# Performance work log

Hardware: AMD Instinct MI355X
Metric: run time of the kernel (lower is better)

The kernel has to match this reference:

```python
import jax, jax.numpy as jnp
import numpy as np

H = 8          # num heads
HD = 64        # head dim
DV = 512       # values_dim
DC = 128       # coords_dim
DI = 512       # att_inner_dim
DF = 2048      # mlp inner dim


def _ln(x, g, b, eps=1e-5):
    mu = jnp.mean(x, -1, keepdims=True)
    var = jnp.mean((x - mu) ** 2, -1, keepdims=True)
    return (x - mu) * jax.lax.rsqrt(var + eps) * g + b


def _rms(x, g, eps=1e-6):
    return x * jax.lax.rsqrt(jnp.mean(x * x, -1, keepdims=True) + eps) * g


def _heads(x):  # b n (h d) -> b h n d
    b, n, _ = x.shape
    return x.reshape(b, n, H, HD).transpose(0, 2, 1, 3)


def setup_inputs() -> dict:
    key = jax.random.key(0)
    ks = iter(jax.random.split(key, 40))
    r = lambda shape, s=0.02: jax.random.normal(next(ks), shape, jnp.float32) * s
    inp = {
        'coords': jax.random.normal(next(ks), (4, 4096, DC), jnp.float32),
        'values': jax.random.normal(next(ks), (4, 4096, DV), jnp.float32),
        'Lv': jax.random.normal(next(ks), (4, 1024, DV), jnp.float32),
        'Lc': jax.random.normal(next(ks), (4, 1024, DC), jnp.float32),
        'lam': jax.random.normal(next(ks), (1,), jnp.float32),
        'lvn_g': jnp.ones((DV,)), 'lvn_b': jnp.zeros((DV,)),
        'lcn_g': jnp.ones((DC,)), 'lcn_b': jnp.zeros((DC,)),
        'ck_w': r((DC, DI)), 'ck_b': jnp.zeros((DI,)), 'ck_g': jnp.ones((DI,)),
        'cq_w': r((DC, DI)), 'cq_b': jnp.zeros((DI,)), 'cq_g': jnp.ones((DI,)),
        'vq_w': r((DV, DI)), 'vq_b': jnp.zeros((DI,)), 'vq_g': jnp.ones((DI,)),
        'vk_w': r((DV, 2 * DI)), 'vk_b': jnp.zeros((2 * DI,)),
        'op_w': r((DI, DV)), 'op_b': jnp.zeros((DV,)),
        'oln_g': jnp.ones((DV,)), 'oln_b': jnp.zeros((DV,)),
        'm1_w': r((DV, DF)), 'm1_b': jnp.zeros((DF,)),
        'm2_w': r((DF, DF)), 'm2_b': jnp.zeros((DF,)),
        'm3_w': r((DF, DV)), 'm3_b': jnp.zeros((DV,)),
    }
    return inp


def reference(coords, values, Lv, Lc, lam, lvn_g, lvn_b, lcn_g, lcn_b,
              ck_w, ck_b, ck_g, cq_w, cq_b, cq_g, vq_w, vq_b, vq_g,
              vk_w, vk_b, op_w, op_b, oln_g, oln_b,
              m1_w, m1_b, m2_w, m2_b, m3_w, m3_b):
    Lv = _ln(Lv, lvn_g, lvn_b)
    Lc = _ln(Lc, lcn_g, lcn_b)
    vk = Lv @ vk_w + vk_b                     # [b, nl, 2*DI]
    v_v, k_v = jnp.split(vk, 2, axis=-1)
    k_c = _rms(Lc @ ck_w + ck_b, ck_g)
    k_c, v_v, k_v = _heads(k_c), _heads(v_v), _heads(k_v)  # [b,h,nl,d]
    q_v = _heads(_rms(values @ vq_w + vq_b, vq_g))         # [b,h,nq,d]
    q_c = _heads(_rms(coords @ cq_w + cq_b, cq_g))
    # dual-score attention
    scores = jnp.einsum('bhnd,bhmd->bhnm', q_c, k_c) \
        + lam[0] * jnp.einsum('bhnd,bhmd->bhnm', q_v, k_v)
    scores = scores / np.float32(np.sqrt(HD))
    attn = jax.nn.softmax(scores, axis=-1)
    V_out = jnp.einsum('bhnm,bhmd->bhnd', attn, v_v)       # [b,h,nq,d]
    b, _, nq, _ = V_out.shape
    V_out = V_out.transpose(0, 2, 1, 3).reshape(b, nq, DI)
    V_out = V_out @ op_w + op_b
    # (LayerNorm, MLP) head: Linear-GELU-Linear-GELU-Linear
    h = _ln(V_out, oln_g, oln_b)
    h = jax.nn.gelu(h @ m1_w + m1_b)
    h = jax.nn.gelu(h @ m2_w + m2_b)
    return h @ m3_w + m3_b
```

## Files before the change

### kernel.cpp

```cpp
#include <hip/hip_runtime.h>
#include <cstdint>
#include <cstddef>

typedef __bf16 bf16_t;
typedef __bf16 bf16x8 __attribute__((ext_vector_type(8)));
typedef __bf16 bf16x4 __attribute__((ext_vector_type(4)));
typedef __bf16 bf16x2 __attribute__((ext_vector_type(2)));
typedef float  f32x4  __attribute__((ext_vector_type(4)));

typedef __attribute__((address_space(1))) void gvoid_t;
typedef __attribute__((address_space(3))) void lvoid_t;

__device__ __forceinline__ f32x4 mfma16(bf16x8 a, bf16x8 b, f32x4 c) {
  return __builtin_amdgcn_mfma_f32_16x16x32_bf16(a, b, c, 0, 0, 0);
}

__device__ __forceinline__ void async_copy16(const void* g, void* l) {
  __builtin_amdgcn_global_load_lds((gvoid_t*)g, (lvoid_t*)l, 16, 0, 0);
}

__device__ __forceinline__ float gelu_tanh(float x) {
  float u = 0.7978845608028654f * (x + 0.044715f * x * x * x);
  float e = exp2f(2.8853900817779268f * u);
  float t = 1.f - 2.f / (e + 1.f);
  return 0.5f * x * (1.f + t);
}

struct TransBatch {
  const float* src[8];
  bf16_t* dst[8];
  int K[8], N[8], bx[8], base[8];
};

__global__ void transpose_batch_kernel(TransBatch d) {
  int id = blockIdx.x;
  int mi = 0;
#pragma unroll
  for (int j = 1; j < 8; j++)
    if (id >= d.base[j]) mi = j;
  int local = id - d.base[mi];
  int bxw = d.bx[mi];
  int n0 = (local % bxw) * 32, k0 = (local / bxw) * 32;
  const float* in = d.src[mi];
  bf16_t* out = d.dst[mi];
  int K = d.K[mi], N = d.N[mi];

  __shared__ float t[32][33];
  int tx = threadIdx.x, ty = threadIdx.y;
#pragma unroll
  for (int i = 0; i < 4; i++)
    t[ty + i * 8][tx] = in[(size_t)(k0 + ty + i * 8) * N + n0 + tx];
  __syncthreads();
#pragma unroll
  for (int i = 0; i < 4; i++)
    out[(size_t)(n0 + ty + i * 8) * K + k0 + tx] = (bf16_t)t[tx][ty + i * 8];
}

__global__ void transpose_v_kernel(const bf16_t* __restrict__ vk, bf16_t* __restrict__ vt) {
  __shared__ bf16_t t[32][33];
  int b = blockIdx.z;
  int d0 = blockIdx.x * 32, m0 = blockIdx.y * 32;
  int tx = threadIdx.x, ty = threadIdx.y;
#pragma unroll
  for (int i = 0; i < 4; i++)
    t[ty + i * 8][tx] = vk[((size_t)b * 1024 + m0 + ty + i * 8) * 1024 + d0 + tx];
  __syncthreads();
#pragma unroll
  for (int i = 0; i < 4; i++)
    vt[((size_t)b * 512 + d0 + ty + i * 8) * 1024 + m0 + tx] = t[tx][ty + i * 8];
}

__global__ void cvt2_bf16_kernel(const float* __restrict__ a, bf16_t* __restrict__ oa, int n4a,
                                 const float* __restrict__ b, bf16_t* __restrict__ ob, int n4b) {
  int i = blockIdx.x * blockDim.x + threadIdx.x;
  const float* s;
  bf16_t* o;
  int j;
  if (i < n4a) { s = a; o = oa; j = i; }
  else { j = i - n4a; if (j >= n4b) return; s = b; o = ob; }
  float4 v = ((const float4*)s)[j];
  bf16x4 r = {(bf16_t)v.x, (bf16_t)v.y, (bf16_t)v.z, (bf16_t)v.w};
  ((bf16x4*)o)[j] = r;
}

template <int D, bool IS_RMS, typename TI>
__global__ __launch_bounds__(256) void rownorm_kernel(
    const TI* __restrict__ x, const float* __restrict__ g,
    const float* __restrict__ bb, bf16_t* __restrict__ out) {
  constexpr int V = D / 64;
  const int row = blockIdx.x * 4 + (threadIdx.x >> 6);
  const int lane = threadIdx.x & 63;
  const size_t base = (size_t)row * D + (size_t)lane * V;
  float v[V];
  if constexpr (sizeof(TI) == 2) {
    bf16x8 xv = *(const bf16x8*)(x + base);
#pragma unroll
    for (int j = 0; j < V; j++) v[j] = (float)xv[j];
  } else if constexpr (V == 8) {
    float4 a = ((const float4*)(x + base))[0];
    float4 b2 = ((const float4*)(x + base))[1];
    v[0] = a.x; v[1] = a.y; v[2] = a.z; v[3] = a.w;
    v[4] = b2.x; v[5] = b2.y; v[6] = b2.z; v[7] = b2.w;
  } else {
    float2 a = *(const float2*)(x + base);
    v[0] = a.x; v[1] = a.y;
  }
  float s = 0.f, s2 = 0.f;
#pragma unroll
  for (int j = 0; j < V; j++) { s += v[j]; s2 += v[j] * v[j]; }
#pragma unroll
  for (int o = 32; o > 0; o >>= 1) { s += __shfl_xor(s, o); s2 += __shfl_xor(s2, o); }
  float mu, rr;
  if constexpr (IS_RMS) {
    mu = 0.f;
    rr = rsqrtf(s2 * (1.f / D) + 1e-6f);
  } else {
    mu = s * (1.f / D);
    rr = rsqrtf(s2 * (1.f / D) - mu * mu + 1e-5f);
  }
  float o[V];
#pragma unroll
  for (int j = 0; j < V; j++) {
    float gv = g[lane * V + j];
    float bv;
    if constexpr (IS_RMS) bv = 0.f; else bv = bb[lane * V + j];
    o[j] = (v[j] - mu) * rr * gv + bv;
  }
  if constexpr (V == 8) {
    bf16x8 ov;
#pragma unroll
    for (int j = 0; j < 8; j++) ov[j] = (bf16_t)o[j];
    *(bf16x8*)(out + base) = ov;
  } else {
    bf16x2 ov;
    ov[0] = (bf16_t)o[0]; ov[1] = (bf16_t)o[1];
    *(bf16x2*)(out + base) = ov;
  }
}

template <int EPI>
__global__ __launch_bounds__(256, 2) void gemm_bt(
    const bf16_t* __restrict__ A, const bf16_t* __restrict__ Bt,
    const float* __restrict__ bias, void* __restrict__ outp,
    int M, int N, int K) {
  __shared__ __align__(16) bf16_t As[128 * 64];
  __shared__ __align__(16) bf16_t Bs[128 * 64];
  const int tid = threadIdx.x;
  const int lane = tid & 63, wv = tid >> 6;
  const int quad = lane >> 4, l16 = lane & 15;
  int nwg = gridDim.x * gridDim.y;
  int bid = blockIdx.y * gridDim.x + blockIdx.x;
  if (!(nwg & 7)) { int cpx = nwg >> 3; bid = (bid & 7) * cpx + (bid >> 3); }
  const int m_base = (bid / gridDim.x) * 128, n_base = (bid % gridDim.x) * 128;
  const int wm = wv & 1, wn = wv >> 1;
  f32x4 acc[4][4] = {};

  for (int k0 = 0; k0 < K; k0 += 64) {
#pragma unroll
    for (int c = 0; c < 4; c++) {
      int p = c * 256 + tid;
      int row = p >> 3;
      int gc = (p & 7) ^ (row & 7);
      async_copy16(&A[(size_t)(m_base + row) * K + k0 + gc * 8], &As[(size_t)p * 8]);
      async_copy16(&Bt[(size_t)(n_base + row) * K + k0 + gc * 8], &Bs[(size_t)p * 8]);
    }
    __syncthreads();
#pragma unroll
    for (int ks = 0; ks < 2; ks++) {
      bf16x8 af[4], bfr[4];
#pragma unroll
      for (int mi = 0; mi < 4; mi++) {
        int r = wm * 64 + mi * 16 + l16;
        int c = (ks * 4 + quad) ^ (r & 7);
        af[mi] = *(const bf16x8*)&As[(size_t)(r * 8 + c) * 8];
      }
#pragma unroll
      for (int ni = 0; ni < 4; ni++) {
        int r = wn * 64 + ni * 16 + l16;
        int c = (ks * 4 + quad) ^ (r & 7);
        bfr[ni] = *(const bf16x8*)&Bs[(size_t)(r * 8 + c) * 8];
      }
#pragma unroll
      for (int mi = 0; mi < 4; mi++)
#pragma unroll
        for (int ni = 0; ni < 4; ni++)
          acc[mi][ni] = mfma16(af[mi], bfr[ni], acc[mi][ni]);
    }
    __syncthreads();
  }

#pragma unroll
  for (int mi = 0; mi < 4; mi++) {
    int m = m_base + wm * 64 + mi * 16 + quad * 4;
#pragma unroll
    for (int ni = 0; ni < 4; ni++) {
      int n = n_base + wn * 64 + ni * 16 + l16;
      float bv = bias[n];
#pragma unroll
      for (int r2 = 0; r2 < 4; r2++) {
        float v = acc[mi][ni][r2] + bv;
        if (EPI == 2) v = gelu_tanh(v);
        if (EPI == 0) ((float*)outp)[(size_t)(m + r2) * N + n] = v;
        else          ((bf16_t*)outp)[(size_t)(m + r2) * N + n] = (bf16_t)v;
      }
    }
  }
}

#define SF __builtin_amdgcn_sched_barrier(0)

template <int EPI>
__global__ __launch_bounds__(512, 2) void gemm256(
    const bf16_t* __restrict__ A, const bf16_t* __restrict__ Bt,
    const float* __restrict__ bias, void* __restrict__ outp,
    int M, int N, int K) {
  __shared__ __align__(16) bf16_t As[2][256 * 64];
  __shared__ __align__(16) bf16_t Bs[2][256 * 64];
  const int tid = threadIdx.x;
  const int lane = tid & 63, wid = tid >> 6;
  const int quad = lane >> 4, l16 = lane & 15, l7 = l16 & 7;
  const int wm = wid >> 2, wn = wid & 3;
  int nwg = gridDim.x * gridDim.y;
  int bid = blockIdx.y * gridDim.x + blockIdx.x;
  if (!(nwg & 7)) { int cpx = nwg >> 3; bid = (bid & 7) * cpx + (bid >> 3); }
  const int m_base = (bid / gridDim.x) * 256, n_base = (bid % gridDim.x) * 256;
  const int nit = K >> 7;

  f32x4 acc[8][4] = {};

  const bf16_t* aB[2]; const bf16_t* bB[2];
#pragma unroll
  for (int ks = 0; ks < 2; ks++) {
    aB[ks] = &As[0][0] + (wm * 128 + l16) * 64 + (((ks * 4 + quad) ^ l7)) * 8;
    bB[ks] = &Bs[0][0] + (wn * 64 + l16) * 64 + (((ks * 4 + quad) ^ l7)) * 8;
  }
  auto ldA = [&](int buf, int rg, bf16x8 (&af)[2][2]) {
#pragma unroll
    for (int mi = 0; mi < 2; mi++)
#pragma unroll
      for (int ks = 0; ks < 2; ks++)
        af[mi][ks] = *(const bf16x8*)(aB[ks] + buf * 16384 + rg * 2048 + mi * 1024);
  };
  auto ldB = [&](int buf, bf16x8 (&bfr)[4][2]) {
#pragma unroll
    for (int cf = 0; cf < 4; cf++)
#pragma unroll
      for (int ks = 0; ks < 2; ks++)
        bfr[cf][ks] = *(const bf16x8*)(bB[ks] + buf * 16384 + cf * 1024);
  };
  auto mm = [&](int rg, bf16x8 (&a)[2][2], bf16x8 (&b)[4][2]) {
#pragma unroll
    for (int ks = 0; ks < 2; ks++)
#pragma unroll
      for (int mi = 0; mi < 2; mi++)
#pragma unroll
        for (int cf = 0; cf < 4; cf++)
          acc[rg * 2 + mi][cf] = mfma16(a[mi][ks], b[cf][ks], acc[rg * 2 + mi][cf]);
  };

  const int rr = tid >> 3;
  const int cb = ((tid & 7) ^ (rr & 7)) * 16;
  const char* pa00 = (const char*)A + 2 * ((size_t)(m_base + 0 + rr) * K) + cb;
  const char* pa01 = (const char*)A + 2 * ((size_t)(m_base + 64 + rr) * K) + cb;
  const char* pa10 = (const char*)A + 2 * ((size_t)(m_base + 128 + rr) * K) + cb;
  const char* pa11 = (const char*)A + 2 * ((size_t)(m_base + 192 + rr) * K) + cb;
  const char* pb00 = (const char*)Bt + 2 * ((size_t)(n_base + 0 + rr) * K) + cb;
  const char* pb01 = (const char*)Bt + 2 * ((size_t)(n_base + 64 + rr) * K) + cb;
  const char* pb10 = (const char*)Bt + 2 * ((size_t)(n_base + 128 + rr) * K) + cb;
  const char* pb11 = (const char*)Bt + 2 * ((size_t)(n_base + 192 + rr) * K) + cb;
  bf16_t* dA0 = &As[0][0] + tid * 8;
  bf16_t* dB0 = &Bs[0][0] + tid * 8;
  auto stage = [&](const char*& p0, const char*& p1, bf16_t* d0) {
    async_copy16(p0, d0);
    async_copy16(p1, d0 + 4096);
    p0 += 128; p1 += 128;
  };

  stage(pb00, pb01, dB0);
  stage(pb10, pb11, dB0 + 8192);
  stage(pa00, pa01, dA0);
  stage(pa10, pa11, dA0 + 8192);
  stage(pb00, pb01, dB0 + 16384);
  stage(pb10, pb11, dB0 + 16384 + 8192);
  stage(pa00, pa01, dA0 + 16384);
  asm volatile("s_waitcnt vmcnt(6)" ::: "memory");
  SF; __builtin_amdgcn_s_barrier(); SF;

  bf16x8 af0[2][2], af1[2][2], bfr[4][2];
  ldB(0, bfr); ldA(0, 0, af0);

  for (int it = 0; it < nit; ++it) {
    ldA(0, 1, af1);
    stage(pa10, pa11, dA0 + 16384 + 8192);
    SF; asm volatile("s_waitcnt lgkmcnt(4)" ::: "memory"); SF;
    __builtin_amdgcn_s_setprio(1); mm(0, af0, bfr); __builtin_amdgcn_s_setprio(0);
    SF; __builtin_amdgcn_s_barrier(); SF;
    ldA(0, 2, af0);
    stage(pb00, pb01, dB0);
    SF; asm volatile("s_waitcnt lgkmcnt(4)" ::: "memory"); SF;
    __builtin_amdgcn_s_setprio(1); mm(1, af1, bfr); __builtin_amdgcn_s_setprio(0);
    SF; __builtin_amdgcn_s_barrier(); SF;
    ldA(0, 3, af1);
    stage(pb10, pb11, dB0 + 8192);
    SF; asm volatile("s_waitcnt lgkmcnt(4)" ::: "memory"); SF;
    __builtin_amdgcn_s_setprio(1); mm(2, af0, bfr); __builtin_amdgcn_s_setprio(0);
    SF; asm volatile("s_waitcnt vmcnt(4) lgkmcnt(0)" ::: "memory");
    __builtin_amdgcn_s_barrier(); SF;
    ldA(1, 0, af0);
    stage(pa00, pa01, dA0);
    SF;
    __builtin_amdgcn_s_setprio(1); mm(3, af1, bfr); __builtin_amdgcn_s_setprio(0);
    SF;
    ldB(1, bfr);
    SF; __builtin_amdgcn_s_barrier(); SF;
    ldA(1, 1, af1);
    stage(pa10, pa11, dA0 + 8192);
    SF; asm volatile("s_waitcnt lgkmcnt(4)" ::: "memory"); SF;
    __builtin_amdgcn_s_setprio(1); mm(0, af0, bfr); __builtin_amdgcn_s_setprio(0);
    SF; __builtin_amdgcn_s_barrier(); SF;
    ldA(1, 2, af0);
    stage(pb00, pb01, dB0 + 16384);
    SF; asm volatile("s_waitcnt lgkmcnt(4)" ::: "memory"); SF;
    __builtin_amdgcn_s_setprio(1); mm(1, af1, bfr); __builtin_amdgcn_s_setprio(0);
    SF; __builtin_amdgcn_s_barrier(); SF;
    ldA(1, 3, af1);
    stage(pb10, pb11, dB0 + 16384 + 8192);
    SF; asm volatile("s_waitcnt lgkmcnt(4)" ::: "memory"); SF;
    __builtin_amdgcn_s_setprio(1); mm(2, af0, bfr); __builtin_amdgcn_s_setprio(0);
    SF; asm volatile("s_waitcnt vmcnt(4) lgkmcnt(0)" ::: "memory");
    __builtin_amdgcn_s_barrier(); SF;
    ldA(0, 0, af0);
    stage(pa00, pa01, dA0 + 16384);
    SF;
    __builtin_amdgcn_s_setprio(1); mm(3, af1, bfr); __builtin_amdgcn_s_setprio(0);
    SF;
    ldB(0, bfr);
    SF; __builtin_amdgcn_s_barrier(); SF;
  }
  asm volatile("s_waitcnt vmcnt(0) lgkmcnt(0)" ::: "memory");

#pragma unroll
  for (int rf = 0; rf < 8; rf++) {
    int m = m_base + wm * 128 + rf * 16 + quad * 4;
#pragma unroll
    for (int cf = 0; cf < 4; cf++) {
      int n = n_base + wn * 64 + cf * 16 + l16;
      float bv = bias[n];
#pragma unroll
      for (int r2 = 0; r2 < 4; r2++) {
        float v = acc[rf][cf][r2] + bv;
        if (EPI == 2) v = gelu_tanh(v);
        if (EPI == 0) ((float*)outp)[(size_t)(m + r2) * N + n] = v;
        else          ((bf16_t*)outp)[(size_t)(m + r2) * N + n] = (bf16_t)v;
      }
    }
  }
}

template <int EPI>
__global__ __launch_bounds__(256, 2) void gemm64(
    const bf16_t* __restrict__ A, const bf16_t* __restrict__ Bt,
    const float* __restrict__ bias, void* __restrict__ outp,
    int M, int N, int K) {
  __shared__ __align__(16) bf16_t As[64 * 32];
  __shared__ __align__(16) bf16_t Bs[128 * 32];
  const int tid = threadIdx.x;
  const int lane = tid & 63, wv = tid >> 6;
  const int quad = lane >> 4, l16 = lane & 15;
  const int m_base = blockIdx.y * 64, n_base = blockIdx.x * 128;
  const int wm = wv & 1, wn = wv >> 1;
  f32x4 acc[2][4] = {};

  for (int k0 = 0; k0 < K; k0 += 32) {
    {
      int p = tid;
      int row = p >> 2;
      int kc = (p & 3) ^ ((row >> 1) & 3);
      async_copy16(&A[(size_t)(m_base + row) * K + k0 + kc * 8], &As[(size_t)p * 8]);
    }
#pragma unroll
    for (int c = 0; c < 2; c++) {
      int p = c * 256 + tid;
      int row = p >> 2;
      int kc = (p & 3) ^ ((row >> 1) & 3);
      async_copy16(&Bt[(size_t)(n_base + row) * K + k0 + kc * 8], &Bs[(size_t)p * 8]);
    }
    __syncthreads();
    bf16x8 af[2], bfr[4];
#pragma unroll
    for (int mi = 0; mi < 2; mi++) {
      int r = wm * 32 + mi * 16 + l16;
      int kc = quad ^ ((r >> 1) & 3);
      af[mi] = *(const bf16x8*)&As[(size_t)(r * 4 + kc) * 8];
    }
#pragma unroll
    for (int ni = 0; ni < 4; ni++) {
      int r = wn * 64 + ni * 16 + l16;
      int kc = quad ^ ((r >> 1) & 3);
      bfr[ni] = *(const bf16x8*)&Bs[(size_t)(r * 4 + kc) * 8];
    }
#pragma unroll
    for (int mi = 0; mi < 2; mi++)
#pragma unroll
      for (int ni = 0; ni < 4; ni++)
        acc[mi][ni] = mfma16(af[mi], bfr[ni], acc[mi][ni]);
    __syncthreads();
  }

#pragma unroll
  for (int mi = 0; mi < 2; mi++) {
    int m = m_base + wm * 32 + mi * 16 + quad * 4;
#pragma unroll
    for (int ni = 0; ni < 4; ni++) {
      int n = n_base + wn * 64 + ni * 16 + l16;
      float bv = bias[n];
#pragma unroll
      for (int r2 = 0; r2 < 4; r2++) {
        float v = acc[mi][ni][r2] + bv;
        if (EPI == 2) v = gelu_tanh(v);
        if (EPI == 0) ((float*)outp)[(size_t)(m + r2) * N + n] = v;
        else          ((bf16_t*)outp)[(size_t)(m + r2) * N + n] = (bf16_t)v;
      }
    }
  }
}

__global__ __launch_bounds__(256, 2) void attn_kernel(
    const bf16_t* __restrict__ qc, const bf16_t* __restrict__ qv,
    const bf16_t* __restrict__ kcb, const bf16_t* __restrict__ vkb,
    const bf16_t* __restrict__ vt, const float* __restrict__ lamp,
    bf16_t* __restrict__ vout) {
  const int b = blockIdx.z, h = blockIdx.y;
  const int tid = threadIdx.x;
  const int lane = tid & 63, wv = tid >> 6;
  const int quad = lane >> 4, l16 = lane & 15;
  const int qrow0 = blockIdx.x * 128 + wv * 32;
  const float SCL = 0.125f * 1.4426950408889634f;
  const float C1 = SCL, C2 = lamp[0] * SCL;

  __shared__ __align__(16) bf16_t kcS[64 * 64];
  __shared__ __align__(16) bf16_t kvS[64 * 64];
  __shared__ __align__(16) bf16_t vtS[64 * 64];
  __shared__ __align__(16) bf16_t sP[4][32 * 64];
  bf16_t* sPw = sP[wv];

  bf16x8 qcf[2][2], qvf[2][2];
#pragma unroll
  for (int mt = 0; mt < 2; mt++)
#pragma unroll
    for (int ks = 0; ks < 2; ks++) {
      size_t o = ((size_t)b * 4096 + qrow0 + mt * 16 + l16) * 512 + h * 64 + ks * 32 + quad * 8;
      qcf[mt][ks] = *(const bf16x8*)&qc[o];
      qvf[mt][ks] = *(const bf16x8*)&qv[o];
    }

  f32x4 O[2][4] = {};
  float ls[2][4] = {};

  for (int kb = 0; kb < 16; kb++) {
#pragma unroll
    for (int i = 0; i < 2; i++) {
      int p = i * 256 + tid;
      int row = p >> 3;
      int gc = (p & 7) ^ (row & 7);
      async_copy16(&kcb[((size_t)b * 1024 + kb * 64 + row) * 512 + h * 64 + gc * 8],
                   &kcS[(size_t)p * 8]);
      async_copy16(&vkb[((size_t)b * 1024 + kb * 64 + row) * 1024 + 512 + h * 64 + gc * 8],
                   &kvS[(size_t)p * 8]);
      async_copy16(&vt[((size_t)((b * 8 + h) * 64) + row) * 1024 + kb * 64 + gc * 8],
                   &vtS[(size_t)p * 8]);
    }
    __syncthreads();

#pragma unroll
    for (int nt = 0; nt < 4; nt++) {
      int krow = nt * 16 + l16;
      int kb8 = krow & 7;
      bf16x8 kc0 = *(const bf16x8*)&kcS[(size_t)(krow * 8 + (quad ^ kb8)) * 8];
      bf16x8 kc1 = *(const bf16x8*)&kcS[(size_t)(krow * 8 + ((4 + quad) ^ kb8)) * 8];
      bf16x8 kv0 = *(const bf16x8*)&kvS[(size_t)(krow * 8 + (quad ^ kb8)) * 8];
      bf16x8 kv1 = *(const bf16x8*)&kvS[(size_t)(krow * 8 + ((4 + quad) ^ kb8)) * 8];
#pragma unroll
      for (int mt = 0; mt < 2; mt++) {
        f32x4 sc = {};
        sc = mfma16(qcf[mt][0], kc0, sc);
        sc = mfma16(qcf[mt][1], kc1, sc);
        f32x4 sv = {};
        sv = mfma16(qvf[mt][0], kv0, sv);
        sv = mfma16(qvf[mt][1], kv1, sv);
#pragma unroll
        for (int r = 0; r < 4; r++) {
          float p = exp2f(sc[r] * C1 + sv[r] * C2);
          ls[mt][r] += p;
          int prow = mt * 16 + quad * 4 + r;
          int col = nt * 16 + l16;
          sPw[prow * 64 + (((col >> 3) ^ (prow & 7)) * 8) + (col & 7)] = (bf16_t)p;
        }
      }
    }
    asm volatile("s_waitcnt lgkmcnt(0)" ::: "memory");

#pragma unroll
    for (int ks2 = 0; ks2 < 2; ks2++) {
      bf16x8 pa[2];
#pragma unroll
      for (int mt = 0; mt < 2; mt++) {
        int prow = mt * 16 + l16;
        pa[mt] = *(const bf16x8*)&sPw[(size_t)(prow * 8 + ((ks2 * 4 + quad) ^ (prow & 7))) * 8];
      }
#pragma unroll
      for (int ntd = 0; ntd < 4; ntd++) {
        int drow = ntd * 16 + l16;
        bf16x8 vb = *(const bf16x8*)&vtS[(size_t)(drow * 8 + ((ks2 * 4 + quad) ^ (drow & 7))) * 8];
        O[0][ntd] = mfma16(pa[0], vb, O[0][ntd]);
        O[1][ntd] = mfma16(pa[1], vb, O[1][ntd]);
      }
    }
    __syncthreads();
  }

#pragma unroll
  for (int mt = 0; mt < 2; mt++) {
    float inv[4];
#pragma unroll
    for (int r = 0; r < 4; r++) {
      float v = ls[mt][r];
      v += __shfl_xor(v, 1);
      v += __shfl_xor(v, 2);
      v += __shfl_xor(v, 4);
      v += __shfl_xor(v, 8);
      inv[r] = 1.f / v;
    }
#pragma unroll
    for (int ntd = 0; ntd < 4; ntd++)
#pragma unroll
      for (int r = 0; r < 4; r++) {
        size_t o = ((size_t)b * 4096 + qrow0 + mt * 16 + quad * 4 + r) * 512 + h * 64 + ntd * 16 + l16;
        vout[o] = (bf16_t)(O[mt][ntd][r] * inv[r]);
      }
  }
}

extern "C" void kernel_launch(void* const* d_in, const int* in_sizes, int n_in,
                              void* d_out, int out_size, void* d_ws, size_t ws_size,
                              hipStream_t stream) {
  (void)in_sizes; (void)n_in; (void)out_size; (void)ws_size;
  const float* coords = (const float*)d_in[0];
  const float* values = (const float*)d_in[1];
  const float* Lv     = (const float*)d_in[2];
  const float* Lc     = (const float*)d_in[3];
  const float* lam    = (const float*)d_in[4];
  const float* lvn_g  = (const float*)d_in[5];
  const float* lvn_b  = (const float*)d_in[6];
  const float* lcn_g  = (const float*)d_in[7];
  const float* lcn_b  = (const float*)d_in[8];
  const float* ck_w = (const float*)d_in[9];  const float* ck_b = (const float*)d_in[10]; const float* ck_g = (const float*)d_in[11];
  const float* cq_w = (const float*)d_in[12]; const float* cq_b = (const float*)d_in[13]; const float* cq_g = (const float*)d_in[14];
  const float* vq_w = (const float*)d_in[15]; const float* vq_b = (const float*)d_in[16]; const float* vq_g = (const float*)d_in[17];
  const float* vk_w = (const float*)d_in[18]; const float* vk_b = (const float*)d_in[19];
  const float* op_w = (const float*)d_in[20]; const float* op_b = (const float*)d_in[21];
  const float* oln_g = (const float*)d_in[22]; const float* oln_b = (const float*)d_in[23];
  const float* m1_w = (const float*)d_in[24]; const float* m1_b = (const float*)d_in[25];
  const float* m2_w = (const float*)d_in[26]; const float* m2_b = (const float*)d_in[27];
  const float* m3_w = (const float*)d_in[28]; const float* m3_b = (const float*)d_in[29];

  char* ws = (char*)d_ws;
  size_t off = 0;
  auto alloc = [&](size_t bytes) { void* p = ws + off; off += (bytes + 255) & ~(size_t)255; return p; };

  bf16_t* wt_m1 = (bf16_t*)alloc((size_t)512 * 2048 * 2);
  bf16_t* wt_m2 = (bf16_t*)alloc((size_t)2048 * 2048 * 2);
  bf16_t* wt_m3 = (bf16_t*)alloc((size_t)2048 * 512 * 2);
  bf16_t* scr0  = (bf16_t*)alloc((size_t)16384 * 512 * 4);
  bf16_t* qv_bf = (bf16_t*)alloc((size_t)16384 * 512 * 2);
  bf16_t* qc_bf = (bf16_t*)alloc((size_t)16384 * 512 * 2);
  bf16_t* voutb = (bf16_t*)alloc((size_t)16384 * 512 * 2);
  bf16_t* h0    = (bf16_t*)alloc((size_t)16384 * 512 * 2);
  bf16_t* h1    = (bf16_t*)alloc((size_t)16384 * 2048 * 2);
  bf16_t* h2    = (bf16_t*)alloc((size_t)16384 * 2048 * 2);

  size_t ov = (size_t)((char*)h1 - ws);
  auto oalloc = [&](size_t bytes) { void* p = ws + ov; ov += (bytes + 255) & ~(size_t)255; return p; };
  bf16_t* wt_vk = (bf16_t*)oalloc((size_t)1024 * 512 * 2);
  bf16_t* wt_ck = (bf16_t*)oalloc((size_t)512 * 128 * 2);
  bf16_t* wt_cq = (bf16_t*)oalloc((size_t)512 * 128 * 2);
  bf16_t* wt_vq = (bf16_t*)oalloc((size_t)512 * 512 * 2);
  bf16_t* wt_op = (bf16_t*)oalloc((size_t)512 * 512 * 2);
  bf16_t* lv_ln = (bf16_t*)oalloc((size_t)4096 * 512 * 2);
  bf16_t* lc_ln = (bf16_t*)oalloc((size_t)4096 * 128 * 2);
  bf16_t* vkob  = (bf16_t*)oalloc((size_t)4096 * 1024 * 2);
  bf16_t* kc_b  = (bf16_t*)oalloc((size_t)4096 * 512 * 2);
  bf16_t* kc_bf = (bf16_t*)oalloc((size_t)4096 * 512 * 2);
  bf16_t* val_bf= (bf16_t*)oalloc((size_t)16384 * 512 * 2);
  bf16_t* crd_bf= (bf16_t*)oalloc((size_t)16384 * 128 * 2);
  bf16_t* vt    = (bf16_t*)oalloc((size_t)4 * 512 * 1024 * 2);

  TransBatch tb8;
  const float* srcs[8] = {vk_w, ck_w, cq_w, vq_w, op_w, m1_w, m2_w, m3_w};
  bf16_t* dsts[8] = {wt_vk, wt_ck, wt_cq, wt_vq, wt_op, wt_m1, wt_m2, wt_m3};
  int Ks[8] = {512, 128, 128, 512, 512, 512, 2048, 2048};
  int Ns[8] = {1024, 512, 512, 512, 512, 2048, 2048, 512};
  int cum = 0;
  for (int i = 0; i < 8; i++) {
    tb8.src[i] = srcs[i]; tb8.dst[i] = dsts[i];
    tb8.K[i] = Ks[i]; tb8.N[i] = Ns[i];
    tb8.bx[i] = Ns[i] / 32;
    tb8.base[i] = cum;
    cum += (Ns[i] / 32) * (Ks[i] / 32);
  }
  transpose_batch_kernel<<<cum, dim3(32, 8), 0, stream>>>(tb8);

  cvt2_bf16_kernel<<<(16384 * 512 / 4 + 16384 * 128 / 4 + 255) / 256, 256, 0, stream>>>(
      values, val_bf, 16384 * 512 / 4, coords, crd_bf, 16384 * 128 / 4);

  rownorm_kernel<512, false, float><<<1024, 256, 0, stream>>>(Lv, lvn_g, lvn_b, lv_ln);
  rownorm_kernel<128, false, float><<<1024, 256, 0, stream>>>(Lc, lcn_g, lcn_b, lc_ln);

  gemm_bt<1><<<dim3(8, 32), 256, 0, stream>>>(lv_ln, wt_vk, vk_b, vkob, 4096, 1024, 512);
  gemm64<1><<<dim3(4, 64), 256, 0, stream>>>(lc_ln, wt_ck, ck_b, kc_b, 4096, 512, 128);
  rownorm_kernel<512, true, bf16_t><<<1024, 256, 0, stream>>>(kc_b, ck_g, nullptr, kc_bf);

  gemm_bt<1><<<dim3(4, 128), 256, 0, stream>>>(val_bf, wt_vq, vq_b, scr0, 16384, 512, 512);
  rownorm_kernel<512, true, bf16_t><<<4096, 256, 0, stream>>>(scr0, vq_g, nullptr, qv_bf);
  gemm64<1><<<dim3(4, 256), 256, 0, stream>>>(crd_bf, wt_cq, cq_b, scr0, 16384, 512, 128);
  rownorm_kernel<512, true, bf16_t><<<4096, 256, 0, stream>>>(scr0, cq_g, nullptr, qc_bf);

  transpose_v_kernel<<<dim3(16, 32, 4), dim3(32, 8), 0, stream>>>(vkob, vt);

  attn_kernel<<<dim3(32, 8, 4), 256, 0, stream>>>(qc_bf, qv_bf, kc_bf, vkob, vt, lam, voutb);

  gemm_bt<1><<<dim3(4, 128), 256, 0, stream>>>(voutb, wt_op, op_b, scr0, 16384, 512, 512);
  rownorm_kernel<512, false, bf16_t><<<4096, 256, 0, stream>>>(scr0, oln_g, oln_b, h0);

  gemm256<2><<<dim3(8, 64), 512, 0, stream>>>(h0, wt_m1, m1_b, h1, 16384, 2048, 512);
  gemm256<2><<<dim3(8, 64), 512, 0, stream>>>(h1, wt_m2, m2_b, h2, 16384, 2048, 2048);
  gemm_bt<0><<<dim3(4, 128), 256, 0, stream>>>(h2, wt_m3, m3_b, (float*)d_out, 16384, 512, 2048);
}
```

Measured before the change: 582.8 us.

## Restructure GEMM main loop to two barriers per half-iteration with paired A fragments

Reorganizes the software-pipelined GEMM main loop so each K-half issues B and two A fragment loads together, then runs two MFMA groups before a barrier. This cuts the barriers per half-iteration from four to two and moves the A-stage issue into the loop start. The cost is shallower prefetch overlap: more LDS reads are waited on (lgkmcnt(0)) between MFMA groups, and global stages are issued in pairs.

```diff
diff --git a/kernel.cpp b/kernel.cpp
--- a/kernel.cpp
+++ b/kernel.cpp
@@ -282,60 +282,46 @@
   stage(pa10, pa11, dA0 + 8192);
   stage(pb00, pb01, dB0 + 16384);
   stage(pb10, pb11, dB0 + 16384 + 8192);
-  stage(pa00, pa01, dA0 + 16384);
-  asm volatile("s_waitcnt vmcnt(6)" ::: "memory");
+  asm volatile("s_waitcnt vmcnt(4)" ::: "memory");
   SF; __builtin_amdgcn_s_barrier(); SF;
 
-  bf16x8 af0[2][2], af1[2][2], bfr[4][2];
-  ldB(0, bfr); ldA(0, 0, af0);
+  bf16x8 aP[2][2], aQ[2][2], bfr[4][2];
 
   for (int it = 0; it < nit; ++it) {
-    ldA(0, 1, af1);
+    ldB(0, bfr); ldA(0, 0, aP); ldA(0, 1, aQ);
+    stage(pa00, pa01, dA0 + 16384);
     stage(pa10, pa11, dA0 + 16384 + 8192);
     SF; asm volatile("s_waitcnt lgkmcnt(4)" ::: "memory"); SF;
-    __builtin_amdgcn_s_setprio(1); mm(0, af0, bfr); __builtin_amdgcn_s_setprio(0);
+    __builtin_amdgcn_s_setprio(1); mm(0, aP, bfr); __builtin_amdgcn_s_setprio(0);
+    SF; asm volatile("s_waitcnt lgkmcnt(0)" ::: "memory"); SF;
+    __builtin_amdgcn_s_setprio(1); mm(1, aQ, bfr); __builtin_amdgcn_s_setprio(0);
     SF; __builtin_amdgcn_s_barrier(); SF;
-    ldA(0, 2, af0);
+    ldA(0, 2, aP); ldA(0, 3, aQ);
     stage(pb00, pb01, dB0);
-    SF; asm volatile("s_waitcnt lgkmcnt(4)" ::: "memory"); SF;
-    __builtin_amdgcn_s_setprio(1); mm(1, af1, bfr); __builtin_amdgcn_s_setprio(0);
-    SF; __builtin_amdgcn_s_barrier(); SF;
-    ldA(0, 3, af1);
     stage(pb10, pb11, dB0 + 8192);
     SF; asm volatile("s_waitcnt lgkmcnt(4)" ::: "memory"); SF;
-    __builtin_amdgcn_s_setprio(1); mm(2, af0, bfr); __builtin_amdgcn_s_setprio(0);
-    SF; asm volatile("s_waitcnt vmcnt(4) lgkmcnt(0)" ::: "memory");
+    __builtin_amdgcn_s_setprio(1); mm(2, aP, bfr); __builtin_amdgcn_s_setprio(0);
+    SF; asm volatile("s_waitcnt lgkmcnt(0)" ::: "memory"); SF;
+    __builtin_amdgcn_s_setprio(1); mm(3, aQ, bfr); __builtin_amdgcn_s_setprio(0);
+    SF; asm volatile("s_waitcnt vmcnt(4)" ::: "memory");
     __builtin_amdgcn_s_barrier(); SF;
-    ldA(1, 0, af0);
+    ldB(1, bfr); ldA(1, 0, aP); ldA(1, 1, aQ);
     stage(pa00, pa01, dA0);
-    SF;
-    __builtin_amdgcn_s_setprio(1); mm(3, af1, bfr); __builtin_amdgcn_s_setprio(0);
-    SF;
-    ldB(1, bfr);
-    SF; __builtin_amdgcn_s_barrier(); SF;
-    ldA(1, 1, af1);
     stage(pa10, pa11, dA0 + 8192);
     SF; asm volatile("s_waitcnt lgkmcnt(4)" ::: "memory"); SF;
-    __builtin_amdgcn_s_setprio(1); mm(0, af0, bfr); __builtin_amdgcn_s_setprio(0);
+    __builtin_amdgcn_s_setprio(1); mm(0, aP, bfr); __builtin_amdgcn_s_setprio(0);
+    SF; asm volatile("s_waitcnt lgkmcnt(0)" ::: "memory"); SF;
+    __builtin_amdgcn_s_setprio(1); mm(1, aQ, bfr); __builtin_amdgcn_s_setprio(0);
     SF; __builtin_amdgcn_s_barrier(); SF;
-    ldA(1, 2, af0);
+    ldA(1, 2, aP); ldA(1, 3, aQ);
     stage(pb00, pb01, dB0 + 16384);
-    SF; asm volatile("s_waitcnt lgkmcnt(4)" ::: "memory"); SF;
-    __builtin_amdgcn_s_setprio(1); mm(1, af1, bfr); __builtin_amdgcn_s_setprio(0);
-    SF; __builtin_amdgcn_s_barrier(); SF;
-    ldA(1, 3, af1);
     stage(pb10, pb11, dB0 + 16384 + 8192);
     SF; asm volatile("s_waitcnt lgkmcnt(4)" ::: "memory"); SF;
-    __builtin_amdgcn_s_setprio(1); mm(2, af0, bfr); __builtin_amdgcn_s_setprio(0);
-    SF; asm volatile("s_waitcnt vmcnt(4) lgkmcnt(0)" ::: "memory");
+    __builtin_amdgcn_s_setprio(1); mm(2, aP, bfr); __builtin_amdgcn_s_setprio(0);
+    SF; asm volatile("s_waitcnt lgkmcnt(0)" ::: "memory"); SF;
+    __builtin_amdgcn_s_setprio(1); mm(3, aQ, bfr); __builtin_amdgcn_s_setprio(0);
+    SF; asm volatile("s_waitcnt vmcnt(4)" ::: "memory");
     __builtin_amdgcn_s_barrier(); SF;
-    ldA(0, 0, af0);
-    stage(pa00, pa01, dA0 + 16384);
-    SF;
-    __builtin_amdgcn_s_setprio(1); mm(3, af1, bfr); __builtin_amdgcn_s_setprio(0);
-    SF;
-    ldB(0, bfr);
-    SF; __builtin_amdgcn_s_barrier(); SF;
   }
   asm volatile("s_waitcnt vmcnt(0) lgkmcnt(0)" ::: "memory");
 
```

New measurement: 597.1 us. 2.4% more time.
